# Optimization experiments

Measured on AMD Instinct MI355X. Metric: run time of the kernel, lower is better.

## Reference

```python
import jax, jax.numpy as jnp
import numpy as np

ALPHA = 10.0
BETA = 0.05
FAR_DELTA = 1e10  # matches torch 10000000000.0 padding for the last delta


def sdf_to_density(signed_distance, alpha, beta):
    s = -signed_distance
    return jnp.where(
        s <= 0,
        alpha * (0.5 * jnp.exp(s / beta)),
        alpha * (1.0 - 0.5 * jnp.exp(-s / beta)),
    )


def setup_inputs() -> dict:
    key = jax.random.key(0)
    k1, k2, k3 = jax.random.split(key, 3)
    R, N = 65536, 128
    distance = jax.random.normal(k1, (R, N), dtype=jnp.float32)  # SDF values
    color = jax.random.uniform(k2, (R, N, 3), dtype=jnp.float32)
    # per-ray sorted sample depths in [2, 6] (near/far)
    t = jax.random.uniform(k3, (R, N), dtype=jnp.float32)
    depth_values = jnp.sort(2.0 + 4.0 * t, axis=-1)
    return {"distance": distance, "color": color, "depth_values": depth_values}


def reference(distance, color, depth_values):
    # deltas: [R, N], last delta padded with a huge value
    deltas = jnp.concatenate(
        [depth_values[:, 1:] - depth_values[:, :-1],
         jnp.full_like(depth_values[:, :1], FAR_DELTA)],
        axis=-1,
    )
    density = sdf_to_density(distance, ALPHA, BETA)  # [R, N]
    d = density * deltas  # [R, N]
    # transmittance: exp(-cumsum of previous densities), exclusive scan
    trans = jnp.exp(-jnp.concatenate(
        [jnp.zeros_like(d[:, :1]), jnp.cumsum(d[:, :-1], axis=-1)], axis=-1))
    weights = (1.0 - jnp.exp(-d)) * trans  # [R, N]
    out_color = jnp.sum(weights[..., None] * color, axis=-2)  # [R, 3]
    geometry = jnp.zeros_like(color)  # faithful to geometry_color = zeros_like(color)
    return out_color, geometry
```

## Files before the change

### kernel.cpp

```cpp
#include <hip/hip_runtime.h>

#define ALPHA     10.0f
#define INV_BETA  20.0f
#define FAR_DELTA 1e10f
#define NSAMP     128

__global__ __launch_bounds__(256) void volsdf_render(
    const float* __restrict__ dist,
    const float* __restrict__ color,
    const float* __restrict__ depth,
    float*       __restrict__ out,
    int R)
{
    const int lane = threadIdx.x & 63;
    const int wave = threadIdx.x >> 6;
    const int ray  = blockIdx.x * 4 + wave;
    if (ray >= R) return;

    const size_t rbase = (size_t)ray * NSAMP;

    float2 di = ((const float2*)(dist  + rbase))[lane];
    float2 dp = ((const float2*)(depth + rbase))[lane];

    float dp_next = __shfl_down(dp.x, 1);
    float delta0  = dp.y - dp.x;
    float delta1  = (lane == 63) ? FAR_DELTA : (dp_next - dp.y);

    float s0 = -di.x, s1 = -di.y;
    float e0 = __expf(-fabsf(s0) * INV_BETA);
    float e1 = __expf(-fabsf(s1) * INV_BETA);
    float dens0 = (s0 <= 0.f) ? (0.5f * ALPHA * e0) : (ALPHA * (1.f - 0.5f * e0));
    float dens1 = (s1 <= 0.f) ? (0.5f * ALPHA * e1) : (ALPHA * (1.f - 0.5f * e1));

    float d0 = dens0 * delta0;
    float d1 = dens1 * delta1;

    float local = d0 + d1;
    float incl  = local;
    #pragma unroll
    for (int off = 1; off < 64; off <<= 1) {
        float v = __shfl_up(incl, off);
        if (lane >= off) incl += v;
    }
    float base = __shfl_up(incl, 1);
    if (lane == 0) base = 0.f;

    float t0 = __expf(-base);
    float t1 = __expf(-(base + d0));
    float w0 = (1.f - __expf(-d0)) * t0;
    float w1 = (1.f - __expf(-d1)) * t1;

    const float* cp = color + rbase * 3 + (size_t)lane * 6;
    float2 c01 = ((const float2*)cp)[0];
    float2 c23 = ((const float2*)cp)[1];
    float2 c45 = ((const float2*)cp)[2];

    float ar = w0 * c01.x + w1 * c23.y;
    float ag = w0 * c01.y + w1 * c45.x;
    float ab = w0 * c23.x + w1 * c45.y;

    #pragma unroll
    for (int off = 32; off > 0; off >>= 1) {
        ar += __shfl_down(ar, off);
        ag += __shfl_down(ag, off);
        ab += __shfl_down(ab, off);
    }
    if (lane == 0) {
        out[(size_t)ray * 3 + 0] = ar;
        out[(size_t)ray * 3 + 1] = ag;
        out[(size_t)ray * 3 + 2] = ab;
    }

    float* geo = out + (size_t)R * 3 + rbase * 3 + (size_t)lane * 6;
    float2 z = make_float2(0.f, 0.f);
    ((float2*)geo)[0] = z;
    ((float2*)geo)[1] = z;
    ((float2*)geo)[2] = z;
}

extern "C" void kernel_launch(void* const* d_in, const int* in_sizes, int n_in,
                              void* d_out, int out_size, void* d_ws, size_t ws_size,
                              hipStream_t stream) {
    const float* dist  = (const float*)d_in[0];
    const float* color = (const float*)d_in[1];
    const float* depth = (const float*)d_in[2];
    float* out = (float*)d_out;

    const int R = in_sizes[0] / NSAMP;
    const int blocks = (R + 3) / 4;

    hipLaunchKernelGGL(volsdf_render, dim3(blocks), dim3(256), 0, stream,
                       dist, color, depth, out, R);
}
```

Baseline: 222.9 us.

## Process two rays per wavefront with float4 loads and 32-lane scans

Each 64-lane wave now handles two rays, one per 32-lane half. Each lane loads four samples with float4 vector loads for distance, depth and color, and the geometry zero-fill is written as float4 stores. The scan and reduction run over 32 lanes instead of 64, and colors are loaded up front to overlap with the compute. This widens memory transactions and cuts shuffle steps per sample, at the cost of more registers per thread. The zero-fill writes a full ray pair without checking whether the second ray is in bounds, which is only safe when R is even.

```diff
diff --git a/kernel.cpp b/kernel.cpp
--- a/kernel.cpp
+++ b/kernel.cpp
@@ -4,6 +4,12 @@
 #define INV_BETA  20.0f
 #define FAR_DELTA 1e10f
 #define NSAMP     128
+
+__device__ __forceinline__ float laplace_density(float sdf) {
+    float s = -sdf;
+    float e = __expf(-fabsf(s) * INV_BETA);
+    return (s <= 0.f) ? (0.5f * ALPHA * e) : (ALPHA * (1.f - 0.5f * e));
+}
 
 __global__ __launch_bounds__(256) void volsdf_render(
     const float* __restrict__ dist,
@@ -12,70 +18,71 @@
     float*       __restrict__ out,
     int R)
 {
-    const int lane = threadIdx.x & 63;
-    const int wave = threadIdx.x >> 6;
-    const int ray  = blockIdx.x * 4 + wave;
+    const int lane   = threadIdx.x & 63;
+    const int waveId = threadIdx.x >> 6;
+    const int sub    = lane & 31;
+    const int half   = lane >> 5;
+    const int rayPair = blockIdx.x * 4 + waveId;
+    const int ray     = rayPair * 2 + half;
     if (ray >= R) return;
 
     const size_t rbase = (size_t)ray * NSAMP;
 
-    float2 di = ((const float2*)(dist  + rbase))[lane];
-    float2 dp = ((const float2*)(depth + rbase))[lane];
+    float4 di = ((const float4*)(dist  + rbase))[sub];
+    float4 dp = ((const float4*)(depth + rbase))[sub];
+    const float* cp = color + rbase * 3 + (size_t)sub * 12;
+    float4 c0 = ((const float4*)cp)[0];
+    float4 c1 = ((const float4*)cp)[1];
+    float4 c2 = ((const float4*)cp)[2];
 
-    float dp_next = __shfl_down(dp.x, 1);
-    float delta0  = dp.y - dp.x;
-    float delta1  = (lane == 63) ? FAR_DELTA : (dp_next - dp.y);
+    float* geo = out + (size_t)R * 3 + (size_t)rayPair * 768;
+    float4 z4 = make_float4(0.f, 0.f, 0.f, 0.f);
+    ((float4*)geo)[lane]       = z4;
+    ((float4*)geo)[64  + lane] = z4;
+    ((float4*)geo)[128 + lane] = z4;
 
-    float s0 = -di.x, s1 = -di.y;
-    float e0 = __expf(-fabsf(s0) * INV_BETA);
-    float e1 = __expf(-fabsf(s1) * INV_BETA);
-    float dens0 = (s0 <= 0.f) ? (0.5f * ALPHA * e0) : (ALPHA * (1.f - 0.5f * e0));
-    float dens1 = (s1 <= 0.f) ? (0.5f * ALPHA * e1) : (ALPHA * (1.f - 0.5f * e1));
+    float nx  = __shfl_down(dp.x, 1, 32);
+    float dl0 = dp.y - dp.x;
+    float dl1 = dp.z - dp.y;
+    float dl2 = dp.w - dp.z;
+    float dl3 = (sub == 31) ? FAR_DELTA : (nx - dp.w);
 
-    float d0 = dens0 * delta0;
-    float d1 = dens1 * delta1;
+    float d0 = laplace_density(di.x) * dl0;
+    float d1 = laplace_density(di.y) * dl1;
+    float d2 = laplace_density(di.z) * dl2;
+    float d3 = laplace_density(di.w) * dl3;
 
-    float local = d0 + d1;
+    float local = (d0 + d1) + (d2 + d3);
     float incl  = local;
     #pragma unroll
-    for (int off = 1; off < 64; off <<= 1) {
-        float v = __shfl_up(incl, off);
-        if (lane >= off) incl += v;
+    for (int off = 1; off < 32; off <<= 1) {
+        float v = __shfl_up(incl, off, 32);
+        if (sub >= off) incl += v;
     }
-    float base = __shfl_up(incl, 1);
-    if (lane == 0) base = 0.f;
+    float base = __shfl_up(incl, 1, 32);
+    if (sub == 0) base = 0.f;
 
-    float t0 = __expf(-base);
-    float t1 = __expf(-(base + d0));
-    float w0 = (1.f - __expf(-d0)) * t0;
-    float w1 = (1.f - __expf(-d1)) * t1;
+    float p1 = base + d0, p2 = p1 + d1, p3 = p2 + d2;
+    float w0 = (1.f - __expf(-d0)) * __expf(-base);
+    float w1 = (1.f - __expf(-d1)) * __expf(-p1);
+    float w2 = (1.f - __expf(-d2)) * __expf(-p2);
+    float w3 = (1.f - __expf(-d3)) * __expf(-p3);
 
-    const float* cp = color + rbase * 3 + (size_t)lane * 6;
-    float2 c01 = ((const float2*)cp)[0];
-    float2 c23 = ((const float2*)cp)[1];
-    float2 c45 = ((const float2*)cp)[2];
-
-    float ar = w0 * c01.x + w1 * c23.y;
-    float ag = w0 * c01.y + w1 * c45.x;
-    float ab = w0 * c23.x + w1 * c45.y;
+    float ar = (w0 * c0.x + w1 * c0.w) + (w2 * c1.z + w3 * c2.y);
+    float ag = (w0 * c0.y + w1 * c1.x) + (w2 * c1.w + w3 * c2.z);
+    float ab = (w0 * c0.z + w1 * c1.y) + (w2 * c2.x + w3 * c2.w);
 
     #pragma unroll
-    for (int off = 32; off > 0; off >>= 1) {
-        ar += __shfl_down(ar, off);
-        ag += __shfl_down(ag, off);
-        ab += __shfl_down(ab, off);
+    for (int off = 16; off > 0; off >>= 1) {
+        ar += __shfl_down(ar, off, 32);
+        ag += __shfl_down(ag, off, 32);
+        ab += __shfl_down(ab, off, 32);
     }
-    if (lane == 0) {
+    if (sub == 0) {
         out[(size_t)ray * 3 + 0] = ar;
         out[(size_t)ray * 3 + 1] = ag;
         out[(size_t)ray * 3 + 2] = ab;
     }
-
-    float* geo = out + (size_t)R * 3 + rbase * 3 + (size_t)lane * 6;
-    float2 z = make_float2(0.f, 0.f);
-    ((float2*)geo)[0] = z;
-    ((float2*)geo)[1] = z;
-    ((float2*)geo)[2] = z;
 }
 
 extern "C" void kernel_launch(void* const* d_in, const int* in_sizes, int n_in,
@@ -87,7 +94,7 @@
     float* out = (float*)d_out;
 
     const int R = in_sizes[0] / NSAMP;
-    const int blocks = (R + 3) / 4;
+    const int blocks = (R + 7) / 8;
 
     hipLaunchKernelGGL(volsdf_render, dim3(blocks), dim3(256), 0, stream,
                        dist, color, depth, out, R);
```

Result: no change. 224.2 us (+0.6%).
